# Optimization experiments

Hardware: AMD Instinct MI355X
Metric: run time of the kernel (lower is better)

## Reference

```python
import jax, jax.numpy as jnp
import numpy as np

B = 4096
MAX_ATOMS = 2048  # angles_max_length + 1
EPS = 1e-12


def setup_inputs() -> dict:
    key = jax.random.key(0)
    k1, k2, k3 = jax.random.split(key, 3)
    inp = jax.random.normal(k1, (B, 3 * MAX_ATOMS), dtype=jnp.float32)
    tgt = jax.random.normal(k2, (B, 3 * MAX_ATOMS), dtype=jnp.float32)
    lengths = jax.random.randint(k3, (B,), 1, 2047, dtype=jnp.int32)
    return {"input": inp, "target": tgt, "angles_length": lengths}


def _kabsch_rmsd(inp, tgt, angles_length):
    # [B, 3*N] flat xyz -> [B, N, 3]
    b, three_n = inp.shape
    n_atoms_max = three_n // 3
    x = inp.reshape(b, n_atoms_max, 3)
    y = tgt.reshape(b, n_atoms_max, 3)
    # number of valid atoms per sample = angles_length + 1
    n_valid = (angles_length + 1).astype(x.dtype)  # [B]
    mask = (jnp.arange(n_atoms_max)[None, :] < (angles_length[:, None] + 1))
    mask = mask.astype(x.dtype)[..., None]  # [B, N, 1]
    # masked centroids
    denom = n_valid[:, None, None]
    cx = (x * mask).sum(axis=1, keepdims=True) / denom
    cy = (y * mask).sum(axis=1, keepdims=True) / denom
    xc = (x - cx) * mask
    yc = (y - cy) * mask
    # sum of squared norms of both centered point sets
    ssq = (xc * xc).sum(axis=(1, 2)) + (yc * yc).sum(axis=(1, 2))  # [B]
    # 3x3 cross-covariance per sample
    C = jnp.einsum('bni,bnj->bij', xc, yc)  # [B, 3, 3]
    U, S, Vt = jnp.linalg.svd(C)
    # Kabsch det correction (proper rotation)
    d = jnp.sign(jnp.linalg.det(U) * jnp.linalg.det(Vt))  # [B]
    tr = S[:, 0] + S[:, 1] + d * S[:, 2]
    msd = jnp.maximum(ssq - 2.0 * tr, 0.0) / n_valid
    return jnp.sqrt(msd + EPS)


def reference(input, target, angles_length):
    return _kabsch_rmsd(input, target, angles_length)
```

## Files before the change

kernel.cpp:

```cpp
#include <hip/hip_runtime.h>
#include <math.h>


#define NACC 17

struct F3 { float x, y, z; };

__global__ __launch_bounds__(256, 8) void kabsch_moments_kernel(
    const float* __restrict__ X,
    const float* __restrict__ Y,
    const int* __restrict__ L,
    float* __restrict__ WS,
    int B)
{
    const int row = blockIdx.x;
    const int tid = threadIdx.x;
    const int n = L[row] + 1;

    const F3* __restrict__ Xr = (const F3*)(X + (size_t)row * 6144);
    const F3* __restrict__ Yr = (const F3*)(Y + (size_t)row * 6144);

    float v[NACC];
#pragma unroll
    for (int k = 0; k < NACC; ++k) v[k] = 0.0f;

#pragma unroll
    for (int batch = 0; batch < 2; ++batch) {
        F3 xa[4], ya[4];
        int atom[4];
#pragma unroll
        for (int i = 0; i < 4; ++i) {
            atom[i] = (batch * 4 + i) * 256 + tid;
            xa[i] = Xr[atom[i]];
        }
#pragma unroll
        for (int i = 0; i < 4; ++i) ya[i] = Yr[atom[i]];

#pragma unroll
        for (int i = 0; i < 4; ++i) {
            const float msk = (atom[i] < n) ? 1.0f : 0.0f;
            const float x0 = xa[i].x * msk;
            const float x1 = xa[i].y * msk;
            const float x2 = xa[i].z * msk;
            const float y0 = ya[i].x * msk;
            const float y1 = ya[i].y * msk;
            const float y2 = ya[i].z * msk;
            v[0] += x0; v[1] += x1; v[2] += x2;
            v[3] += y0; v[4] += y1; v[5] += y2;
            v[6] += x0 * x0 + x1 * x1 + x2 * x2;
            v[7] += y0 * y0 + y1 * y1 + y2 * y2;
            v[8]  += x0 * y0; v[9]  += x0 * y1; v[10] += x0 * y2;
            v[11] += x1 * y0; v[12] += x1 * y1; v[13] += x1 * y2;
            v[14] += x2 * y0; v[15] += x2 * y1; v[16] += x2 * y2;
        }
    }

#pragma unroll
    for (int k = 0; k < NACC; ++k) {
        float t = v[k];
        t += __shfl_down(t, 32);
        t += __shfl_down(t, 16);
        t += __shfl_down(t, 8);
        t += __shfl_down(t, 4);
        t += __shfl_down(t, 2);
        t += __shfl_down(t, 1);
        v[k] = t;
    }

    __shared__ float red[4][NACC];
    const int wave = tid >> 6;
    const int lane = tid & 63;
    if (lane == 0) {
#pragma unroll
        for (int k = 0; k < NACC; ++k) red[wave][k] = v[k];
    }
    __syncthreads();

    if (tid < NACC) {
        const float s = red[0][tid] + red[1][tid] + red[2][tid] + red[3][tid];
        WS[(size_t)tid * B + row] = s;
    }
}

__global__ __launch_bounds__(64) void kabsch_eig_kernel(
    const float* __restrict__ WS,
    const int* __restrict__ L,
    float* __restrict__ OUT,
    int B)
{
    const int row = blockIdx.x * 64 + threadIdx.x;
    if (row >= B) return;
    const int n = L[row] + 1;

    double s[NACC];
#pragma unroll
    for (int k = 0; k < NACC; ++k)
        s[k] = (double)WS[(size_t)k * B + row];

    const double inv_n = 1.0 / (double)n;
    const double sx0 = s[0], sx1 = s[1], sx2 = s[2];
    const double sy0 = s[3], sy1 = s[4], sy2 = s[5];
    const double ssq = s[6] + s[7]
        - (sx0 * sx0 + sx1 * sx1 + sx2 * sx2) * inv_n
        - (sy0 * sy0 + sy1 * sy1 + sy2 * sy2) * inv_n;

    double C[3][3];
    C[0][0] = s[8]  - sx0 * sy0 * inv_n;
    C[0][1] = s[9]  - sx0 * sy1 * inv_n;
    C[0][2] = s[10] - sx0 * sy2 * inv_n;
    C[1][0] = s[11] - sx1 * sy0 * inv_n;
    C[1][1] = s[12] - sx1 * sy1 * inv_n;
    C[1][2] = s[13] - sx1 * sy2 * inv_n;
    C[2][0] = s[14] - sx2 * sy0 * inv_n;
    C[2][1] = s[15] - sx2 * sy1 * inv_n;
    C[2][2] = s[16] - sx2 * sy2 * inv_n;

    const double det =
          C[0][0] * (C[1][1] * C[2][2] - C[1][2] * C[2][1])
        - C[0][1] * (C[1][0] * C[2][2] - C[1][2] * C[2][0])
        + C[0][2] * (C[1][0] * C[2][1] - C[1][1] * C[2][0]);

    double A[3][3];
#pragma unroll
    for (int i = 0; i < 3; ++i)
#pragma unroll
        for (int j = 0; j < 3; ++j)
            A[i][j] = C[0][i] * C[0][j] + C[1][i] * C[1][j] + C[2][i] * C[2][j];

    const double q  = (A[0][0] + A[1][1] + A[2][2]) / 3.0;
    const double p1 = A[0][1] * A[0][1] + A[0][2] * A[0][2] + A[1][2] * A[1][2];
    const double a00 = A[0][0] - q, a11 = A[1][1] - q, a22 = A[2][2] - q;
    const double p2 = a00 * a00 + a11 * a11 + a22 * a22 + 2.0 * p1;
    const double p  = sqrt(p2 / 6.0);

    double e1, e2, e3;
    if (p < 1e-30) {
        e1 = e2 = e3 = q;
    } else {
        const double ip = 1.0 / p;
        const double b00 = a00 * ip, b11 = a11 * ip, b22 = a22 * ip;
        const double b01 = A[0][1] * ip, b02 = A[0][2] * ip, b12 = A[1][2] * ip;
        double r = 0.5 * (b00 * (b11 * b22 - b12 * b12)
                        - b01 * (b01 * b22 - b12 * b02)
                        + b02 * (b01 * b12 - b11 * b02));
        r = fmin(1.0, fmax(-1.0, r));
        const double phi = acos(r) / 3.0;
        e1 = q + 2.0 * p * cos(phi);
        e3 = q + 2.0 * p * cos(phi + 2.0 * M_PI / 3.0);
        e2 = 3.0 * q - e1 - e3;
    }

    const double S0 = sqrt(fmax(e1, 0.0));
    const double S1 = sqrt(fmax(e2, 0.0));
    const double S2 = sqrt(fmax(e3, 0.0));
    const double d  = (det > 0.0) ? 1.0 : ((det < 0.0) ? -1.0 : 0.0);
    const double tr = S0 + S1 + d * S2;

    const double msd = fmax(ssq - 2.0 * tr, 0.0) * inv_n;
    OUT[row] = (float)sqrt(msd + 1e-12);
}

extern "C" void kernel_launch(void* const* d_in, const int* in_sizes, int n_in,
                              void* d_out, int out_size, void* d_ws, size_t ws_size,
                              hipStream_t stream) {
    const float* X = (const float*)d_in[0];
    const float* Y = (const float*)d_in[1];
    const int* L = (const int*)d_in[2];
    float* OUT = (float*)d_out;
    float* WS = (float*)d_ws;

    const int B = in_sizes[2];
    kabsch_moments_kernel<<<B, 256, 0, stream>>>(X, Y, L, WS, B);
    kabsch_eig_kernel<<<(B + 63) / 64, 64, 0, stream>>>(WS, L, OUT, B);
}
```

Before: 231.7 us.

## Assign one wave per row and read only valid atoms with float4 prefetch

The moments kernel now maps one 64-lane wave to each sample row instead of a 256-thread block. Each wave loops only over the 256-atom chunks that contain valid atoms, so padded atoms past the per-row length are never read. Loads become three float4 per array per lane, with the next chunk prefetched into registers. The cross-wave shared-memory reduction and its barrier are removed. In exchange, each wave carries a variable-length loop, so long rows finish later than short ones, and there are fewer threads per row to hide memory latency.

Measured after the change: 201.8 us. 12.9% less time.

```diff
diff --git a/kernel.cpp b/kernel.cpp
--- a/kernel.cpp
+++ b/kernel.cpp
@@ -3,48 +3,65 @@
 
 
 #define NACC 17
+#define ROWF 6144
 
-struct F3 { float x, y, z; };
-
-__global__ __launch_bounds__(256, 8) void kabsch_moments_kernel(
+__global__ __launch_bounds__(256) void kabsch_moments_kernel(
     const float* __restrict__ X,
     const float* __restrict__ Y,
     const int* __restrict__ L,
     float* __restrict__ WS,
     int B)
 {
-    const int row = blockIdx.x;
-    const int tid = threadIdx.x;
+    const int gwave = (int)((blockIdx.x * 256u + threadIdx.x) >> 6);
+    const int lane  = threadIdx.x & 63;
+    if (gwave >= B) return;
+    const int row = gwave;
     const int n = L[row] + 1;
+    const int nIter = (n + 255) >> 8;
 
-    const F3* __restrict__ Xr = (const F3*)(X + (size_t)row * 6144);
-    const F3* __restrict__ Yr = (const F3*)(Y + (size_t)row * 6144);
+    const float* gX = X + (size_t)row * ROWF + (size_t)lane * 12;
+    const float* gY = Y + (size_t)row * ROWF + (size_t)lane * 12;
 
     float v[NACC];
 #pragma unroll
     for (int k = 0; k < NACC; ++k) v[k] = 0.0f;
 
+    float4 cx0, cx1, cx2, cy0, cy1, cy2;
+    {
+        const float4* px = (const float4*)gX;
+        const float4* py = (const float4*)gY;
+        cx0 = px[0]; cx1 = px[1]; cx2 = px[2];
+        cy0 = py[0]; cy1 = py[1]; cy2 = py[2];
+    }
+
+    for (int it = 0; it < nIter; ++it) {
+        float4 nx0, nx1, nx2, ny0, ny1, ny2;
+        const bool more = (it + 1 < nIter);
+        if (more) {
+            const float4* px = (const float4*)(gX + (it + 1) * 768);
+            const float4* py = (const float4*)(gY + (it + 1) * 768);
+            nx0 = px[0]; nx1 = px[1]; nx2 = px[2];
+            ny0 = py[0]; ny1 = py[1]; ny2 = py[2];
+        }
+
+        float fx[12], fy[12];
+        fx[0]=cx0.x; fx[1]=cx0.y; fx[2]=cx0.z; fx[3]=cx0.w;
+        fx[4]=cx1.x; fx[5]=cx1.y; fx[6]=cx1.z; fx[7]=cx1.w;
+        fx[8]=cx2.x; fx[9]=cx2.y; fx[10]=cx2.z; fx[11]=cx2.w;
+        fy[0]=cy0.x; fy[1]=cy0.y; fy[2]=cy0.z; fy[3]=cy0.w;
+        fy[4]=cy1.x; fy[5]=cy1.y; fy[6]=cy1.z; fy[7]=cy1.w;
+        fy[8]=cy2.x; fy[9]=cy2.y; fy[10]=cy2.z; fy[11]=cy2.w;
+
+        const int abase = it * 256 + lane * 4;
 #pragma unroll
-    for (int batch = 0; batch < 2; ++batch) {
-        F3 xa[4], ya[4];
-        int atom[4];
-#pragma unroll
-        for (int i = 0; i < 4; ++i) {
-            atom[i] = (batch * 4 + i) * 256 + tid;
-            xa[i] = Xr[atom[i]];
-        }
-#pragma unroll
-        for (int i = 0; i < 4; ++i) ya[i] = Yr[atom[i]];
-
-#pragma unroll
-        for (int i = 0; i < 4; ++i) {
-            const float msk = (atom[i] < n) ? 1.0f : 0.0f;
-            const float x0 = xa[i].x * msk;
-            const float x1 = xa[i].y * msk;
-            const float x2 = xa[i].z * msk;
-            const float y0 = ya[i].x * msk;
-            const float y1 = ya[i].y * msk;
-            const float y2 = ya[i].z * msk;
+        for (int j = 0; j < 4; ++j) {
+            const float msk = (abase + j < n) ? 1.0f : 0.0f;
+            const float x0 = fx[3 * j + 0] * msk;
+            const float x1 = fx[3 * j + 1] * msk;
+            const float x2 = fx[3 * j + 2] * msk;
+            const float y0 = fy[3 * j + 0] * msk;
+            const float y1 = fy[3 * j + 1] * msk;
+            const float y2 = fy[3 * j + 2] * msk;
             v[0] += x0; v[1] += x1; v[2] += x2;
             v[3] += y0; v[4] += y1; v[5] += y2;
             v[6] += x0 * x0 + x1 * x1 + x2 * x2;
@@ -52,6 +69,11 @@
             v[8]  += x0 * y0; v[9]  += x0 * y1; v[10] += x0 * y2;
             v[11] += x1 * y0; v[12] += x1 * y1; v[13] += x1 * y2;
             v[14] += x2 * y0; v[15] += x2 * y1; v[16] += x2 * y2;
+        }
+
+        if (more) {
+            cx0 = nx0; cx1 = nx1; cx2 = nx2;
+            cy0 = ny0; cy1 = ny1; cy2 = ny2;
         }
     }
 
@@ -67,28 +89,20 @@
         v[k] = t;
     }
 
-    __shared__ float red[4][NACC];
-    const int wave = tid >> 6;
-    const int lane = tid & 63;
     if (lane == 0) {
 #pragma unroll
-        for (int k = 0; k < NACC; ++k) red[wave][k] = v[k];
-    }
-    __syncthreads();
-
-    if (tid < NACC) {
-        const float s = red[0][tid] + red[1][tid] + red[2][tid] + red[3][tid];
-        WS[(size_t)tid * B + row] = s;
+        for (int k = 0; k < NACC; ++k)
+            WS[(size_t)k * B + row] = v[k];
     }
 }
 
-__global__ __launch_bounds__(64) void kabsch_eig_kernel(
+__global__ __launch_bounds__(256) void kabsch_eig_kernel(
     const float* __restrict__ WS,
     const int* __restrict__ L,
     float* __restrict__ OUT,
     int B)
 {
-    const int row = blockIdx.x * 64 + threadIdx.x;
+    const int row = blockIdx.x * 256 + threadIdx.x;
     if (row >= B) return;
     const int n = L[row] + 1;
 
@@ -170,6 +184,7 @@
     float* WS = (float*)d_ws;
 
     const int B = in_sizes[2];
-    kabsch_moments_kernel<<<B, 256, 0, stream>>>(X, Y, L, WS, B);
-    kabsch_eig_kernel<<<(B + 63) / 64, 64, 0, stream>>>(WS, L, OUT, B);
+    const int waves_blocks = (B * 64 + 255) / 256;
+    kabsch_moments_kernel<<<waves_blocks, 256, 0, stream>>>(X, Y, L, WS, B);
+    kabsch_eig_kernel<<<(B + 255) / 256, 256, 0, stream>>>(WS, L, OUT, B);
 }
```
